# Optimization experiments

Hardware: AMD Instinct MI355X
Metric: run time of the kernel (lower is better)

## Reference

```python
import jax, jax.numpy as jnp
from jax import lax
import numpy as np

N, C_IN, C_OUT, H, W, D = 16, 32, 64, 128, 128, 5


def setup_inputs() -> dict:
    key = jax.random.key(0)
    k1, k2, k3, k4 = jax.random.split(key, 4)
    x = jax.random.normal(k1, (N, 1, C_IN, H, W), jnp.float32)
    d = jax.random.normal(k2, (N, C_OUT, C_IN, D, D), jnp.float32)
    y = jax.random.normal(k3, (N, C_OUT, 1, H, W), jnp.float32)
    alpha = jax.random.uniform(k4, (N, 1, 1, 1), jnp.float32)
    return {"x": x, "d": d, "y": y, "alpha": alpha, "reg": 1.0}


def _cross_corr(wts, img, pad):
    # out[i, j, u, v] = sum_{h,w} wts[i,h,w] * img[j, h+u-pad, w+v-pad]
    # (valid sums, zero padding). Implements the per-sample full-image conv3d
    # of the torch code (cross-correlation, no kernel flip).
    out = lax.conv_general_dilated(img[:, None], wts[:, None], (1, 1),
                                   [(pad, pad), (pad, pad)])
    return out.transpose(1, 0, 2, 3)  # (Ci_wts, Cj_img, 2*pad+1, 2*pad+1)


def reference(x, d, y, alpha, reg):
    n, _, c_in, h, w = x.shape
    c_out, ds = d.shape[1], d.shape[-1]
    K = c_in * ds * ds
    # Full autocorrelation R[n,c0,c1,a,b] = sum x[c0,h,w]*x[c1,h+a-(ds-1), w+b-(ds-1)]
    R = jax.vmap(lambda xn: _cross_corr(xn, xn, ds - 1))(x[:, 0])  # (n,C,C,2ds-1,2ds-1)
    # Toeplitz block assembly: Q[(c0,p,q),(c1,s,t)] = R[c0,c1, s-p+ds-1, t-q+ds-1]
    shift = jnp.arange(ds)[None, :] - jnp.arange(ds)[:, None] + (ds - 1)  # [p,s]
    Qa = R[:, :, :, shift, :]            # (n,c0,c1,p,s,2ds-1)
    Qb = Qa[..., shift]                  # (n,c0,c1,p,s,q,t)
    Q = Qb.transpose(0, 1, 3, 5, 2, 4, 6).reshape(n, K, K)
    # X^T y: S[n,o,c,u,v] = sum y[o,h,w]*x[c, h+u-p0, w+v-p0], p0=(ds-1)//2
    S = jax.vmap(lambda yn, xn: _cross_corr(yn, xn, (ds - 1) // 2))(y[:, :, 0], x[:, 0])
    P = S.transpose(0, 2, 3, 4, 1).reshape(n, K, c_out)
    # Tikhonov regularization around previous dictionary d
    a = alpha.reshape(n, 1) * (h * w * reg / (ds * ds * c_in))  # (n,1)
    Q = Q + a[:, :, None] * jnp.eye(K, dtype=Q.dtype)
    P = P + a[:, :, None] * d.reshape(n, c_out, K).transpose(0, 2, 1)
    # Batched Cholesky solve: D = Q^{-1} P
    L = jnp.linalg.cholesky(Q)
    z = lax.linalg.triangular_solve(L, P, left_side=True, lower=True)
    Dsol = lax.linalg.triangular_solve(L, z, left_side=True, lower=True, transpose_a=True)
    return Dsol.reshape(n, c_in, ds, ds, c_out).transpose(0, 4, 1, 2, 3)
```

## Files before the change

### kernel.cpp

```cpp
#include <hip/hip_runtime.h>

#define R_SZ    737280
#define Q_SZ    10240000
#define P_SZ    819200
#define LI_SZ   1024000
#define W_SZ    4608000

typedef unsigned short u16;
typedef __attribute__((ext_vector_type(8))) short bf16x8;
typedef __attribute__((ext_vector_type(4))) float f32x4;

#define MFMA16(a, b, c) __builtin_amdgcn_mfma_f32_16x16x32_bf16(a, b, c, 0, 0, 0)

__device__ __forceinline__ float alpha_scale(const float* alpha, const float* reg, int n) {
  return alpha[n] * (16384.0f * reg[0] / 800.0f);
}

__device__ __forceinline__ u16 f2bf(float f) {
  union { float f; unsigned u; } v; v.f = f;
  unsigned r = v.u + 0x7FFFu + ((v.u >> 16) & 1u);
  return (u16)(r >> 16);
}
__device__ __forceinline__ float bf2f(u16 h) {
  union { unsigned u; float f; } v; v.u = ((unsigned)h) << 16; return v.f;
}

__device__ __forceinline__ bf16x8 load8(const u16* p) {
  union { uint4 d; bf16x8 v; } u;
  u.d = *(const uint4*)p;
  return u.v;
}

__device__ __forceinline__ bf16x8 build_frag(const unsigned* w, int s) {
  union { unsigned u[4]; bf16x8 v; } f;
  int b = s >> 1;
  if (s & 1) {
    #pragma unroll
    for (int k = 0; k < 4; ++k) f.u[k] = (w[b + k] >> 16) | (w[b + k + 1] << 16);
  } else {
    #pragma unroll
    for (int k = 0; k < 4; ++k) f.u[k] = w[b + k];
  }
  return f.v;
}

__device__ __forceinline__ void stage_row(u16* slot, int partStride,
                                          const float* __restrict__ img,
                                          int C, int r, bool valid,
                                          int tid, int nthr) {
  for (int idx = tid; idx < C * 16; idx += nthr) {
    int c = idx >> 4, m = idx & 15;
    float v[8];
    if (valid) {
      const float* p = img + ((size_t)c * 128 + r) * 128 + m * 8;
      float4 a = *(const float4*)p;
      float4 b = *(const float4*)(p + 4);
      v[0]=a.x; v[1]=a.y; v[2]=a.z; v[3]=a.w; v[4]=b.x; v[5]=b.y; v[6]=b.z; v[7]=b.w;
    } else {
      #pragma unroll
      for (int k = 0; k < 8; ++k) v[k] = 0.0f;
    }
    union { u16 s[8]; uint2 d[2]; } hh, ll;
    #pragma unroll
    for (int k = 0; k < 8; ++k) {
      u16 h = f2bf(v[k]);
      hh.s[k] = h;
      ll.s[k] = f2bf(v[k] - bf2f(h));
    }
    u16* dh = slot + c * 136 + 4 + m * 8;
    *(uint2*)(dh)     = hh.d[0];
    *(uint2*)(dh + 4) = hh.d[1];
    u16* dl = dh + partStride;
    *(uint2*)(dl)     = ll.d[0];
    *(uint2*)(dl + 4) = ll.d[1];
  }
}

#define SLOT_US 8704
#define PSTR_32 4352
#define YPSTR   8704

__global__ __launch_bounds__(640) void k_corrR_mfma(const float* __restrict__ x,
                                                    float* __restrict__ Rpart) {
  __shared__ __align__(16) u16 lds[5 * SLOT_US];
  int n  = blockIdx.x >> 4;
  int r0 = (blockIdx.x & 15) << 3;
  int tid = threadIdx.x;
  const float* xn = x + (size_t)n * 32 * 128 * 128;

  if (tid < 320) {
    int s = tid / 64, p = (tid >> 5) & 1, c = tid & 31;
    u16* b = lds + s * SLOT_US + p * PSTR_32 + c * 136;
    uint2 z; z.x = 0; z.y = 0;
    *(uint2*)b = z;
    *(uint2*)(b + 132) = z;
  }
  for (int rr = 0; rr < 5; ++rr) {
    int r = r0 + rr;
    stage_row(lds + (r % 5) * SLOT_US, PSTR_32, xn, 32, r, r < 128, tid, 640);
  }

  int wave = tid >> 6, lane = tid & 63;
  int du = wave >> 1, nt = wave & 1;
  int lm = lane & 15, q = lane >> 4;

  f32x4 acc[9][2];
  #pragma unroll
  for (int dvi = 0; dvi < 9; ++dvi)
    #pragma unroll
    for (int mt = 0; mt < 2; ++mt) acc[dvi][mt] = (f32x4){0.f, 0.f, 0.f, 0.f};

  for (int i = r0; i < r0 + 8; ++i) {
    __syncthreads();
    const u16* A  = lds + (i % 5) * SLOT_US;
    const u16* Bp = lds + ((i + du) % 5) * SLOT_US;
    #pragma unroll
    for (int ks = 0; ks < 4; ++ks) {
      int kb = ks * 32 + q * 8;
      bf16x8 af[2][2];
      #pragma unroll
      for (int pa = 0; pa < 2; ++pa)
        #pragma unroll
        for (int mt = 0; mt < 2; ++mt)
          af[pa][mt] = load8(A + pa * PSTR_32 + (mt * 16 + lm) * 136 + 4 + kb);
      #pragma unroll
      for (int pb = 0; pb < 2; ++pb) {
        const u16* wp = Bp + pb * PSTR_32 + (nt * 16 + lm) * 136 + kb;
        uint4 w0 = *(const uint4*)wp;
        uint4 w1 = *(const uint4*)(wp + 8);
        unsigned w[8] = {w0.x, w0.y, w0.z, w0.w, w1.x, w1.y, w1.z, w1.w};
        #pragma unroll
        for (int dvi = 0; dvi < 9; ++dvi) {
          bf16x8 bf = build_frag(w, dvi);
          #pragma unroll
          for (int mt = 0; mt < 2; ++mt)
            #pragma unroll
            for (int pa = 0; pa < 2; ++pa) {
              if (pa == 1 && pb == 1) continue;
              acc[dvi][mt] = MFMA16(af[pa][mt], bf, acc[dvi][mt]);
            }
        }
      }
    }
    __syncthreads();
    if (i + 1 < r0 + 8) {
      int r = i + 5;
      stage_row(lds + (r % 5) * SLOT_US, PSTR_32, xn, 32, r, r < 128, tid, 640);
    }
  }

  float* Rp = Rpart + (size_t)blockIdx.x * 46080;
  #pragma unroll
  for (int dvi = 0; dvi < 9; ++dvi)
    #pragma unroll
    for (int mt = 0; mt < 2; ++mt) {
      float* dst = Rp + (du * 9 + dvi) * 1024 + (nt * 16 + lm) * 32 + mt * 16 + q * 4;
      *(f32x4*)dst = acc[dvi][mt];
    }
}

__global__ void k_reduceR(const float* __restrict__ part, float* __restrict__ R) {
  int idx = blockIdx.x * 256 + threadIdx.x;
  int n = idx / 46080, rem = idx % 46080;
  const float* p = part + (size_t)n * 16 * 46080 + rem;
  float s = 0.0f;
  #pragma unroll
  for (int c = 0; c < 16; ++c) s += p[(size_t)c * 46080];
  R[idx] = s;
}

__global__ __launch_bounds__(640) void k_corrP_mfma(const float* __restrict__ x,
                                                    const float* __restrict__ y,
                                                    float* __restrict__ Ppart) {
  __shared__ __align__(16) u16 xs[5 * SLOT_US];
  __shared__ __align__(16) u16 ys[2 * YPSTR];
  int n  = blockIdx.x >> 4;
  int r0 = (blockIdx.x & 15) << 3;
  int tid = threadIdx.x;
  const float* xn = x + (size_t)n * 32 * 128 * 128;
  const float* yn = y + (size_t)n * 64 * 128 * 128;

  if (tid < 320) {
    int s = tid / 64, p = (tid >> 5) & 1, c = tid & 31;
    u16* b = xs + s * SLOT_US + p * PSTR_32 + c * 136;
    uint2 z; z.x = 0; z.y = 0;
    *(uint2*)b = z;
    *(uint2*)(b + 132) = z;
  }
  for (int rr = -2; rr <= 2; ++rr) {
    int r = r0 + rr;
    stage_row(xs + ((r + 10) % 5) * SLOT_US, PSTR_32, xn, 32, r,
              (r >= 0 && r < 128), tid, 640);
  }
  stage_row(ys, YPSTR, yn, 64, r0, true, tid, 640);

  int wave = tid >> 6, lane = tid & 63;
  int du = (wave >> 1) - 2, mh = wave & 1;
  int lm = lane & 15, q = lane >> 4;

  f32x4 acc[5][2][2];
  #pragma unroll
  for (int dvi = 0; dvi < 5; ++dvi)
    #pragma unroll
    for (int mt = 0; mt < 2; ++mt)
      #pragma unroll
      for (int nt = 0; nt < 2; ++nt)
        acc[dvi][mt][nt] = (f32x4){0.f, 0.f, 0.f, 0.f};

  for (int i = r0; i < r0 + 8; ++i) {
    __syncthreads();
    const u16* Bp = xs + ((i + du + 10) % 5) * SLOT_US;
    #pragma unroll
    for (int ks = 0; ks < 4; ++ks) {
      int kb = ks * 32 + q * 8;
      bf16x8 af[2][2];
      #pragma unroll
      for (int pa = 0; pa < 2; ++pa)
        #pragma unroll
        for (int mt = 0; mt < 2; ++mt)
          af[pa][mt] = load8(ys + pa * YPSTR + (mh * 32 + mt * 16 + lm) * 136 + 4 + kb);
      #pragma unroll
      for (int nt = 0; nt < 2; ++nt)
        #pragma unroll
        for (int pb = 0; pb < 2; ++pb) {
          const u16* wp = Bp + pb * PSTR_32 + (nt * 16 + lm) * 136 + kb;
          uint4 w0 = *(const uint4*)wp;
          uint4 w1 = *(const uint4*)(wp + 8);
          unsigned w[8] = {w0.x, w0.y, w0.z, w0.w, w1.x, w1.y, w1.z, w1.w};
          #pragma unroll
          for (int dvi = 0; dvi < 5; ++dvi) {
            bf16x8 bf = build_frag(w, dvi + 2);
            #pragma unroll
            for (int mt = 0; mt < 2; ++mt)
              #pragma unroll
              for (int pa = 0; pa < 2; ++pa) {
                if (pa == 1 && pb == 1) continue;
                acc[dvi][mt][nt] = MFMA16(af[pa][mt], bf, acc[dvi][mt][nt]);
              }
          }
        }
    }
    __syncthreads();
    if (i + 1 < r0 + 8) {
      int r = i + 3;
      stage_row(xs + ((r + 10) % 5) * SLOT_US, PSTR_32, xn, 32, r,
                (r >= 0 && r < 128), tid, 640);
      stage_row(ys, YPSTR, yn, 64, i + 1, true, tid, 640);
    }
  }

  float* Pp = Ppart + (size_t)blockIdx.x * 51200;
  #pragma unroll
  for (int dvi = 0; dvi < 5; ++dvi)
    #pragma unroll
    for (int mt = 0; mt < 2; ++mt)
      #pragma unroll
      for (int nt = 0; nt < 2; ++nt) {
        float* dst = Pp + ((du + 2) * 5 + dvi) * 2048 + (nt * 16 + lm) * 64
                        + mh * 32 + mt * 16 + q * 4;
        *(f32x4*)dst = acc[dvi][mt][nt];
      }
}

__global__ void k_reduceP(const float* __restrict__ part, const float* __restrict__ d,
                          const float* __restrict__ alpha, const float* __restrict__ reg,
                          float* __restrict__ P) {
  int idx = blockIdx.x * 256 + threadIdx.x;
  int n = idx / 51200, rem = idx % 51200;
  int k = rem >> 6, co = rem & 63;
  int ci = k / 25, ae = k % 25;
  const float* p = part + (size_t)n * 16 * 51200 + (ae * 32 + ci) * 64 + co;
  float s = 0.0f;
  #pragma unroll
  for (int c = 0; c < 16; ++c) s += p[(size_t)c * 51200];
  float a = alpha_scale(alpha, reg, n);
  P[idx] = s + a * d[((size_t)n * 64 + co) * 800 + k];
}

__global__ void k_buildQ(const float* __restrict__ R, float* __restrict__ Q,
                         const float* __restrict__ alpha, const float* __restrict__ reg) {
  int bid = blockIdx.x;
  int n = bid / 800, k1 = bid % 800;
  int c1 = k1 / 25, r1 = k1 % 25, a = r1 / 5, e = r1 % 5;
  float av = alpha_scale(alpha, reg, n);
  const float* Rn = R + (size_t)n * 45 * 1024;
  float* Qrow = Q + ((size_t)n * 800 + k1) * 800;
  for (int k2 = threadIdx.x; k2 < 800; k2 += 256) {
    int c2 = k2 / 25, r2 = k2 % 25, b = r2 / 5, f = r2 % 5;
    int du = b - a, dv = f - e;
    float v = (du >= 0)
      ? Rn[(du * 9 + dv + 4) * 1024 + c2 * 32 + c1]
      : Rn[((-du) * 9 + 4 - dv) * 1024 + c1 * 32 + c2];
    if (k2 == k1) v += av;
    Qrow[k2] = v;
  }
}

#define DS 82

__device__ void diag_factor_invert2(float* As, float* Bs,
                                    float* __restrict__ Ln, float* __restrict__ LnT,
                                    int tid) {
  __shared__ float Dinv_s[16 * 25];
  for (int s = 0; s < 16; ++s) {
    int b = 5 * s;
    float a[5][5], dinv[5];
    #pragma unroll
    for (int ii = 0; ii < 5; ++ii)
      #pragma unroll
      for (int kk = 0; kk <= ii; ++kk) a[ii][kk] = As[(b+ii)*DS + b+kk];
    #pragma unroll
    for (int jj = 0; jj < 5; ++jj) {
      float dd = sqrtf(a[jj][jj]);
      a[jj][jj] = dd; dinv[jj] = 1.0f / dd;
      #pragma unroll
      for (int ii = jj+1; ii < 5; ++ii) a[ii][jj] *= dinv[jj];
      #pragma unroll
      for (int ii = jj+1; ii < 5; ++ii)
        #pragma unroll
        for (int kk = jj+1; kk <= ii; ++kk) a[ii][kk] -= a[ii][jj] * a[kk][jj];
    }
    if (tid < 25) {
      int ii = tid / 5, kk = tid % 5;
      if (kk <= ii) As[(b+ii)*DS + b+kk] = a[ii][kk];
    }
    int m = 75 - b;
    for (int r = tid; r < m; r += 256) {
      int row = b + 5 + r;
      float w[5];
      #pragma unroll
      for (int c = 0; c < 5; ++c) {
        float av2 = As[row*DS + b + c];
        #pragma unroll
        for (int kk = 0; kk < c; ++kk) av2 -= w[kk] * a[c][kk];
        w[c] = av2 * dinv[c];
      }
      #pragma unroll
      for (int c = 0; c < 5; ++c) As[row*DS + b + c] = w[c];
    }
    __syncthreads();
    for (int idx = tid; idx < m*m; idx += 256) {
      int ii = idx / m, kk = idx % m;
      if (kk <= ii) {
        int ri = b+5+ii, rk = b+5+kk;
        float acc2 = As[ri*DS + rk];
        #pragma unroll
        for (int c = 0; c < 5; ++c) acc2 -= As[ri*DS + b+c] * As[rk*DS + b+c];
        As[ri*DS + rk] = acc2;
      }
    }
    __syncthreads();
  }

  if (tid < 16) {
    int i = tid;
    const float* Ab = As + (5*i)*DS + 5*i;
    float L5[5][5], Di[5][5];
    #pragma unroll
    for (int r = 0; r < 5; ++r)
      #pragma unroll
      for (int c = 0; c <= r; ++c) L5[r][c] = Ab[r*DS + c];
    #pragma unroll
    for (int c = 0; c < 5; ++c) {
      #pragma unroll
      for (int r = 0; r < c; ++r) Di[r][c] = 0.0f;
      Di[c][c] = 1.0f / L5[c][c];
      #pragma unroll
      for (int r = c+1; r < 5; ++r) {
        float sacc = 0.0f;
        #pragma unroll
        for (int k = c; k < r; ++k) sacc += L5[r][k] * Di[k][c];
        Di[r][c] = -sacc * (1.0f / L5[r][r]);
      }
    }
    #pragma unroll
    for (int r = 0; r < 5; ++r)
      #pragma unroll
      for (int c = 0; c < 5; ++c) Dinv_s[i*25 + r*5 + c] = Di[r][c];
  }
  __syncthreads();

  if (tid < 80) {
    int j = tid;
    for (int i = 0; i < 16; ++i) {
      float bv[5];
      #pragma unroll
      for (int r = 0; r < 5; ++r) bv[r] = (5*i + r == j) ? 1.0f : 0.0f;
      const float* Arow = As + (5*i)*DS;
      #pragma unroll 5
      for (int k = 0; k < 5*i; ++k) {
        float xc = Bs[k*DS + j];
        #pragma unroll
        for (int r = 0; r < 5; ++r) bv[r] -= Arow[r*DS + k] * xc;
      }
      #pragma unroll
      for (int r = 0; r < 5; ++r) {
        float v = 0.0f;
        #pragma unroll
        for (int c = 0; c <= r; ++c) v += Dinv_s[i*25 + r*5 + c] * bv[c];
        Bs[(5*i + r)*DS + j] = v;
      }
    }
  }
  __syncthreads();
  for (int idx = tid; idx < 6400; idx += 256) {
    int r = idx / 80, c = idx % 80;
    float v = (r >= c) ? Bs[r*DS + c] : 0.0f;
    Ln[idx] = v;
    LnT[c*80 + r] = v;
  }
}

__global__ __launch_bounds__(256) void k_diag0(const float* __restrict__ Q,
                                               float* __restrict__ Linv,
                                               float* __restrict__ LinvT) {
  __shared__ float As[80*DS];
  __shared__ float Bs[80*DS];
  int n = blockIdx.x, tid = threadIdx.x;
  const float* Qn = Q + (size_t)n * 640000;
  for (int idx = tid; idx < 6400; idx += 256) {
    int r = idx / 80, c = idx % 80;
    As[r*DS + c] = Qn[r*800 + c];
  }
  __syncthreads();
  diag_factor_invert2(As, Bs, Linv + (size_t)n*10*6400, LinvT + (size_t)n*10*6400, tid);
}

__global__ __launch_bounds__(256) void k_chol_step(float* __restrict__ Q,
                                                   float* __restrict__ Linv,
                                                   float* __restrict__ LinvT,
                                                   float* __restrict__ Wrm,
                                                   float* __restrict__ Wcm,
                                                   int t) {
  int nt = 9 - t;
  int T = nt * (nt + 1) / 2;
  int n = blockIdx.x / T;
  int rr = blockIdx.x % T;
  int i = 0;
  while (rr >= i + 1) { rr -= i + 1; ++i; }
  int j = rr;
  int bi = t + 1 + i, bj = t + 1 + j;

  __shared__ float Ls[80*DS];
  __shared__ float Aa[80*DS];
  __shared__ float W1[80*DS];
  __shared__ float W2[80*DS];
  int tid = threadIdx.x, tc = tid & 15, tr = tid >> 4;
  float* Qn = Q + (size_t)n * 640000;
  const float* Ln = Linv + ((size_t)n*10 + t) * 6400;

  for (int idx = tid; idx < 6400; idx += 256) {
    int r = idx / 80, c = idx % 80;
    Ls[r*DS + c] = Ln[idx];
    Aa[r*DS + c] = Qn[(size_t)(80*bi + r)*800 + 80*t + c];
  }
  __syncthreads();

  float acc[5][5];
  #pragma unroll
  for (int a = 0; a < 5; ++a)
    #pragma unroll
    for (int b = 0; b < 5; ++b) acc[a][b] = 0.0f;
  for (int k = 0; k < 80; ++k) {
    float av[5], bv[5];
    #pragma unroll
    for (int dd = 0; dd < 5; ++dd) { av[dd] = Aa[(5*tr+dd)*DS + k]; bv[dd] = Ls[(5*tc+dd)*DS + k]; }
    #pragma unroll
    for (int a = 0; a < 5; ++a)
      #pragma unroll
      for (int b = 0; b < 5; ++b) acc[a][b] += av[a] * bv[b];
  }
  #pragma unroll
  for (int a = 0; a < 5; ++a)
    #pragma unroll
    for (int b = 0; b < 5; ++b) W1[(5*tr+a)*DS + 5*tc+b] = acc[a][b];
  if (i == j) {
    int p = t*9 - t*(t-1)/2 + i;
    size_t base = ((size_t)n*45 + p) * 6400;
    #pragma unroll
    for (int a = 0; a < 5; ++a)
      #pragma unroll
      for (int b = 0; b < 5; ++b) {
        Wrm[base + (5*tr+a)*80 + 5*tc+b] = acc[a][b];
        Wcm[base + (5*tc+b)*80 + 5*tr+a] = acc[a][b];
      }
  }
  __syncthreads();

  const float* Wia = W1;
  const float* Wjb = W1;
  if (i != j) {
    for (int idx = tid; idx < 6400; idx += 256) {
      int r = idx / 80, c = idx % 80;
      Aa[r*DS + c] = Qn[(size_t)(80*bj + r)*800 + 80*t + c];
    }
    __syncthreads();
    #pragma unroll
    for (int a = 0; a < 5; ++a)
      #pragma unroll
      for (int b = 0; b < 5; ++b) acc[a][b] = 0.0f;
    for (int k = 0; k < 80; ++k) {
      float av[5], bv[5];
      #pragma unroll
      for (int dd = 0; dd < 5; ++dd) { av[dd] = Aa[(5*tr+dd)*DS + k]; bv[dd] = Ls[(5*tc+dd)*DS + k]; }
      #pragma unroll
      for (int a = 0; a < 5; ++a)
        #pragma unroll
        for (int b = 0; b < 5; ++b) acc[a][b] += av[a] * bv[b];
    }
    #pragma unroll
    for (int a = 0; a < 5; ++a)
      #pragma unroll
      for (int b = 0; b < 5; ++b) W2[(5*tr+a)*DS + 5*tc+b] = acc[a][b];
    Wjb = W2;
    __syncthreads();
  }

  for (int idx = tid; idx < 6400; idx += 256) {
    int r = idx / 80, c = idx % 80;
    Aa[r*DS + c] = Qn[(size_t)(80*bi + r)*800 + 80*bj + c];
  }
  __syncthreads();

  #pragma unroll
  for (int a = 0; a < 5; ++a)
    #pragma unroll
    for (int b = 0; b < 5; ++b) acc[a][b] = 0.0f;
  for (int k = 0; k < 80; ++k) {
    float av[5], bv[5];
    #pragma unroll
    for (int dd = 0; dd < 5; ++dd) { av[dd] = Wia[(5*tr+dd)*DS + k]; bv[dd] = Wjb[(5*tc+dd)*DS + k]; }
    #pragma unroll
    for (int a = 0; a < 5; ++a)
      #pragma unroll
      for (int b = 0; b < 5; ++b) acc[a][b] += av[a] * bv[b];
  }

  bool special = (i == 0 && j == 0);
  if (!special) {
    #pragma unroll
    for (int a = 0; a < 5; ++a)
      #pragma unroll
      for (int b = 0; b < 5; ++b)
        Qn[(size_t)(80*bi + 5*tr+a)*800 + 80*bj + 5*tc+b] =
          Aa[(5*tr+a)*DS + 5*tc+b] - acc[a][b];
  } else {
    #pragma unroll
    for (int a = 0; a < 5; ++a)
      #pragma unroll
      for (int b = 0; b < 5; ++b)
        Aa[(5*tr+a)*DS + 5*tc+b] -= acc[a][b];
    __syncthreads();
    diag_factor_invert2(Aa, Ls,
                        Linv  + ((size_t)n*10 + t + 1) * 6400,
                        LinvT + ((size_t)n*10 + t + 1) * 6400, tid);
  }
}


__device__ __forceinline__ void seg80c(const float* __restrict__ M, int i,
                                       const float2 (&zc)[80],
                                       float& a0, float& a1) {
  const float* Mi = M + i * 80;
  float4 A[8];
  #pragma unroll
  for (int q = 0; q < 8; ++q) A[q] = *(const float4*)(Mi + 4 * q);
  #pragma unroll
  for (int h = 0; h < 20; ++h) {
    float4 v = A[h & 7];
    if (h + 8 < 20) A[h & 7] = *(const float4*)(Mi + 4 * (h + 8));
    a0 += v.x * zc[4*h].x;     a1 += v.x * zc[4*h].y;
    a0 += v.y * zc[4*h + 1].x; a1 += v.y * zc[4*h + 1].y;
    a0 += v.z * zc[4*h + 2].x; a1 += v.z * zc[4*h + 2].y;
    a0 += v.w * zc[4*h + 3].x; a1 += v.w * zc[4*h + 3].y;
  }
}

__global__ __launch_bounds__(320, 2) void k_solve(const float* __restrict__ Linv,
                                                  const float* __restrict__ LinvT,
                                                  const float* __restrict__ Wrm,
                                                  const float* __restrict__ Wcm,
                                                  const float* __restrict__ P,
                                                  float* __restrict__ out) {
  __shared__ __align__(16) float z2[4 * 800 * 2];
  int n   = blockIdx.x >> 3;
  int qg8 = (blockIdx.x & 7) << 3;
  int tid = threadIdx.x;
  int i   = tid % 80;
  int cp  = tid / 80;
  const float* Lb  = Linv  + (size_t)n * 10 * 6400;
  const float* LTb = LinvT + (size_t)n * 10 * 6400;
  const float* Wr  = Wrm + (size_t)n * 45 * 6400;
  const float* Wc  = Wcm + (size_t)n * 45 * 6400;

  for (int idx = tid; idx < 6400; idx += 320) {
    int k = idx >> 3, cc = idx & 7;
    z2[((cc >> 1) * 800 + k) * 2 + (cc & 1)] =
        P[((size_t)n * 800 + k) * 64 + qg8 + cc];
  }

  float2 zc[80];

  for (int t = 0; t < 10; ++t) {
    __syncthreads();
    int zb = (cp * 800 + 80 * t) * 2;
    #pragma unroll
    for (int m = 0; m < 40; ++m) {
      float4 v = *(const float4*)&z2[zb + 4 * m];
      zc[2*m]     = make_float2(v.x, v.y);
      zc[2*m + 1] = make_float2(v.z, v.w);
    }
    float a0 = 0.f, a1 = 0.f;
    seg80c(Lb + t * 6400, i, zc, a0, a1);
    __syncthreads();
    *(float2*)&z2[(cp * 800 + 80 * t + i) * 2] = make_float2(a0, a1);
    __syncthreads();
    #pragma unroll
    for (int m = 0; m < 40; ++m) {
      float4 v = *(const float4*)&z2[zb + 4 * m];
      zc[2*m]     = make_float2(v.x, v.y);
      zc[2*m + 1] = make_float2(v.z, v.w);
    }
    int nseg = 9 - t;
    const float* Mc = Wr + (size_t)(t * 9 - t * (t - 1) / 2) * 6400;
    for (int s = 0; s < nseg; ++s) {
      float b0 = 0.f, b1 = 0.f;
      seg80c(Mc + (size_t)s * 6400, i, zc, b0, b1);
      float2* zp = (float2*)&z2[(cp * 800 + 80 * (t + 1 + s) + i) * 2];
      float2 v = *zp; v.x -= b0; v.y -= b1; *zp = v;
    }
  }

  for (int t = 9; t >= 0; --t) {
    __syncthreads();
    int zb = (cp * 800 + 80 * t) * 2;
    #pragma unroll
    for (int m = 0; m < 40; ++m) {
      float4 v = *(const float4*)&z2[zb + 4 * m];
      zc[2*m]     = make_float2(v.x, v.y);
      zc[2*m + 1] = make_float2(v.z, v.w);
    }
    float a0 = 0.f, a1 = 0.f;
    seg80c(LTb + t * 6400, i, zc, a0, a1);
    __syncthreads();
    *(float2*)&z2[(cp * 800 + 80 * t + i) * 2] = make_float2(a0, a1);
    __syncthreads();
    #pragma unroll
    for (int m = 0; m < 40; ++m) {
      float4 v = *(const float4*)&z2[zb + 4 * m];
      zc[2*m]     = make_float2(v.x, v.y);
      zc[2*m + 1] = make_float2(v.z, v.w);
    }
    for (int u = t - 1; u >= 0; --u) {
      int p = u * 9 - u * (u - 1) / 2 + (t - u - 1);
      float b0 = 0.f, b1 = 0.f;
      seg80c(Wc + (size_t)p * 6400, i, zc, b0, b1);
      float2* zp = (float2*)&z2[(cp * 800 + 80 * u + i) * 2];
      float2 v = *zp; v.x -= b0; v.y -= b1; *zp = v;
    }
  }

  __syncthreads();
  for (int idx = tid; idx < 6400; idx += 320) {
    int c = idx / 800, k = idx % 800;
    out[((size_t)n * 64 + qg8 + c) * 800 + k] =
        z2[((c >> 1) * 800 + k) * 2 + (c & 1)];
  }
}

extern "C" void kernel_launch(void* const* d_in, const int* in_sizes, int n_in,
                              void* d_out, int out_size, void* d_ws, size_t ws_size,
                              hipStream_t stream) {
  const float* x     = (const float*)d_in[0];
  const float* d     = (const float*)d_in[1];
  const float* y     = (const float*)d_in[2];
  const float* alpha = (const float*)d_in[3];
  const float* reg   = (const float*)d_in[4];
  float* out = (float*)d_out;
  float* ws  = (float*)d_ws;

  float* R    = ws;
  float* Q    = R + R_SZ;
  float* P    = Q + Q_SZ;
  float* Li   = P + P_SZ;
  float* part = Li + LI_SZ;
  float* LiT  = part;
  float* Wrm  = part + LI_SZ;
  float* Wcm  = Wrm + W_SZ;

  k_corrR_mfma<<<256, 640, 0, stream>>>(x, part);
  k_reduceR<<<R_SZ / 256, 256, 0, stream>>>(part, R);
  k_corrP_mfma<<<256, 640, 0, stream>>>(x, y, part);
  k_reduceP<<<P_SZ / 256, 256, 0, stream>>>(part, d, alpha, reg, P);
  k_buildQ<<<16 * 800, 256, 0, stream>>>(R, Q, alpha, reg);

  k_diag0<<<16, 256, 0, stream>>>(Q, Li, LiT);
  for (int t = 0; t < 9; ++t) {
    int nt = 9 - t;
    k_chol_step<<<16 * nt * (nt + 1) / 2, 256, 0, stream>>>(Q, Li, LiT, Wrm, Wcm, t);
  }

  k_solve<<<16 * 8, 320, 0, stream>>>(Li, LiT, Wrm, Wcm, P, out);
}
```

Measured before the change: 1.484 ms.

## Prefetch next block across segments in solve and split columns over more blocks

The triangular solve kernel now carries its register prefetch buffer across matrix segments, so the first rows of the next 80x80 block load while the current block is being consumed. Before, each segment began with a cold load. The grid is also doubled to 256 blocks of 160 threads, each handling 4 right-hand-side columns instead of 8, with half the shared memory per block. This gives more parallel blocks across the device, but each column group now streams the same L-inverse and W matrices again, doubling the total reads of those matrices.

```diff
diff --git a/kernel.cpp b/kernel.cpp
--- a/kernel.cpp
+++ b/kernel.cpp
@@ -557,18 +557,21 @@
   }
 }
 
-
-__device__ __forceinline__ void seg80c(const float* __restrict__ M, int i,
+#define ZS 20
+
+__device__ __forceinline__ void seg80p(const float* __restrict__ Mcur, int i,
+                                       const float* __restrict__ Mnext,
+                                       float4 (&A)[8],
                                        const float2 (&zc)[80],
                                        float& a0, float& a1) {
-  const float* Mi = M + i * 80;
-  float4 A[8];
-  #pragma unroll
-  for (int q = 0; q < 8; ++q) A[q] = *(const float4*)(Mi + 4 * q);
+  const float* Ci = Mcur + i * 80;
+  const float* Ni = Mnext + i * 80;
   #pragma unroll
   for (int h = 0; h < 20; ++h) {
     float4 v = A[h & 7];
-    if (h + 8 < 20) A[h & 7] = *(const float4*)(Mi + 4 * (h + 8));
+    if (h < 12)      A[h & 7]  = *(const float4*)(Ci + 4 * (h + 8));
+    else if (h < 16) A[h - 8]  = *(const float4*)(Ni + 4 * (h - 8));
+    else             A[h - 16] = *(const float4*)(Ni + 4 * (h - 16));
     a0 += v.x * zc[4*h].x;     a1 += v.x * zc[4*h].y;
     a0 += v.y * zc[4*h + 1].x; a1 += v.y * zc[4*h + 1].y;
     a0 += v.z * zc[4*h + 2].x; a1 += v.z * zc[4*h + 2].y;
@@ -576,15 +579,15 @@
   }
 }
 
-__global__ __launch_bounds__(320, 2) void k_solve(const float* __restrict__ Linv,
+__global__ __launch_bounds__(160, 1) void k_solve(const float* __restrict__ Linv,
                                                   const float* __restrict__ LinvT,
                                                   const float* __restrict__ Wrm,
                                                   const float* __restrict__ Wcm,
                                                   const float* __restrict__ P,
                                                   float* __restrict__ out) {
-  __shared__ __align__(16) float z2[4 * 800 * 2];
-  int n   = blockIdx.x >> 3;
-  int qg8 = (blockIdx.x & 7) << 3;
+  __shared__ __align__(16) float z2[2 * 800 * 2];
+  int n   = blockIdx.x >> 4;
+  int qg4 = (blockIdx.x & 15) << 2;
   int tid = threadIdx.x;
   int i   = tid % 80;
   int cp  = tid / 80;
@@ -593,13 +596,19 @@
   const float* Wr  = Wrm + (size_t)n * 45 * 6400;
   const float* Wc  = Wcm + (size_t)n * 45 * 6400;
 
-  for (int idx = tid; idx < 6400; idx += 320) {
-    int k = idx >> 3, cc = idx & 7;
+  for (int idx = tid; idx < 3200; idx += 160) {
+    int k = idx >> 2, cc = idx & 3;
     z2[((cc >> 1) * 800 + k) * 2 + (cc & 1)] =
-        P[((size_t)n * 800 + k) * 64 + qg8 + cc];
+        P[((size_t)n * 800 + k) * 64 + qg4 + cc];
   }
 
   float2 zc[80];
+  float4 A[8];
+  {
+    const float* Mi = Lb + i * 80;
+    #pragma unroll
+    for (int q = 0; q < 8; ++q) A[q] = *(const float4*)(Mi + 4 * q);
+  }
 
   for (int t = 0; t < 10; ++t) {
     __syncthreads();
@@ -610,8 +619,12 @@
       zc[2*m]     = make_float2(v.x, v.y);
       zc[2*m + 1] = make_float2(v.z, v.w);
     }
+    int nseg = 9 - t;
+    const float* Mc = Wr + (size_t)(t * 9 - t * (t - 1) / 2) * 6400;
+    const float* nxt = (nseg > 0) ? Mc
+                      : (t < 9 ? Lb + (t + 1) * 6400 : LTb + 9 * 6400);
     float a0 = 0.f, a1 = 0.f;
-    seg80c(Lb + t * 6400, i, zc, a0, a1);
+    seg80p(Lb + t * 6400, i, nxt, A, zc, a0, a1);
     __syncthreads();
     *(float2*)&z2[(cp * 800 + 80 * t + i) * 2] = make_float2(a0, a1);
     __syncthreads();
@@ -621,11 +634,11 @@
       zc[2*m]     = make_float2(v.x, v.y);
       zc[2*m + 1] = make_float2(v.z, v.w);
     }
-    int nseg = 9 - t;
-    const float* Mc = Wr + (size_t)(t * 9 - t * (t - 1) / 2) * 6400;
     for (int s = 0; s < nseg; ++s) {
+      const float* nx2 = (s + 1 < nseg) ? Mc + (size_t)(s + 1) * 6400
+                                        : Lb + (t + 1) * 6400;
       float b0 = 0.f, b1 = 0.f;
-      seg80c(Mc + (size_t)s * 6400, i, zc, b0, b1);
+      seg80p(Mc + (size_t)s * 6400, i, nx2, A, zc, b0, b1);
       float2* zp = (float2*)&z2[(cp * 800 + 80 * (t + 1 + s) + i) * 2];
       float2 v = *zp; v.x -= b0; v.y -= b1; *zp = v;
     }
@@ -640,8 +653,13 @@
       zc[2*m]     = make_float2(v.x, v.y);
       zc[2*m + 1] = make_float2(v.z, v.w);
     }
+    const float* nxt;
+    if (t > 0) {
+      int p0 = (t - 1) * 9 - (t - 1) * (t - 2) / 2;
+      nxt = Wc + (size_t)p0 * 6400;
+    } else nxt = Lb;
     float a0 = 0.f, a1 = 0.f;
-    seg80c(LTb + t * 6400, i, zc, a0, a1);
+    seg80p(LTb + t * 6400, i, nxt, A, zc, a0, a1);
     __syncthreads();
     *(float2*)&z2[(cp * 800 + 80 * t + i) * 2] = make_float2(a0, a1);
     __syncthreads();
@@ -653,17 +671,22 @@
     }
     for (int u = t - 1; u >= 0; --u) {
       int p = u * 9 - u * (u - 1) / 2 + (t - u - 1);
+      const float* nx2;
+      if (u > 0) {
+        int pn = (u - 1) * 9 - (u - 1) * (u - 2) / 2 + (t - u);
+        nx2 = Wc + (size_t)pn * 6400;
+      } else nx2 = (t > 0) ? LTb + (t - 1) * 6400 : Lb;
       float b0 = 0.f, b1 = 0.f;
-      seg80c(Wc + (size_t)p * 6400, i, zc, b0, b1);
+      seg80p(Wc + (size_t)p * 6400, i, nx2, A, zc, b0, b1);
       float2* zp = (float2*)&z2[(cp * 800 + 80 * u + i) * 2];
       float2 v = *zp; v.x -= b0; v.y -= b1; *zp = v;
     }
   }
 
   __syncthreads();
-  for (int idx = tid; idx < 6400; idx += 320) {
+  for (int idx = tid; idx < 3200; idx += 160) {
     int c = idx / 800, k = idx % 800;
-    out[((size_t)n * 64 + qg8 + c) * 800 + k] =
+    out[((size_t)n * 64 + qg4 + c) * 800 + k] =
         z2[((c >> 1) * 800 + k) * 2 + (c & 1)];
   }
 }
@@ -700,5 +723,5 @@
     k_chol_step<<<16 * nt * (nt + 1) / 2, 256, 0, stream>>>(Q, Li, LiT, Wrm, Wcm, t);
   }
 
-  k_solve<<<16 * 8, 320, 0, stream>>>(Li, LiT, Wrm, Wcm, P, out);
-}
+  k_solve<<<16 * 16, 160, 0, stream>>>(Li, LiT, Wrm, Wcm, P, out);
+}
```

Result: faster. 1.409 ms (-5.1%).
